# Kernel optimization log

Measured on AMD Instinct MI355X. Metric: run time of the kernel, lower is better.

Reference implementation:

```python
import jax, jax.numpy as jnp
import numpy as np

B = 4096
D = 2048            # in_out_dim
HALF = D // 2       # 1024
MID = 4096          # mid_dim
N_HIDDEN = 5 - 1    # hidden - 1 square layers
MASK = 1            # mask_config


def setup_inputs() -> dict:
    key = jax.random.key(0)
    ks = jax.random.split(key, 8)
    s_in = 1.0 / np.sqrt(HALF)
    s_mid = 1.0 / np.sqrt(MID)
    return {
        "x": jax.random.normal(ks[0], (B, D), dtype=jnp.float32),
        "log_det_J": jnp.zeros((), dtype=jnp.float32),
        "W_in": jax.random.uniform(ks[1], (HALF, MID), jnp.float32, -s_in, s_in),
        "b_in": jax.random.uniform(ks[2], (MID,), jnp.float32, -s_in, s_in),
        "W_h": jax.random.uniform(ks[3], (N_HIDDEN, MID, MID), jnp.float32, -s_mid, s_mid),
        "b_h": jax.random.uniform(ks[4], (N_HIDDEN, MID), jnp.float32, -s_mid, s_mid),
        "W_out": jax.random.uniform(ks[5], (MID, HALF), jnp.float32, -s_mid, s_mid),
        "b_out": jax.random.uniform(ks[6], (HALF,), jnp.float32, -s_mid, s_mid),
    }


def reference(x, log_det_J, W_in, b_in, W_h, b_h, W_out, b_out):
    # reverse=False (sampling mode), mask_config=1
    xr = x.reshape(B, HALF, 2)
    if MASK:
        x1, x2 = xr[:, :, 0], xr[:, :, 1]
    else:
        x1, x2 = xr[:, :, 1], xr[:, :, 0]
    # MLP on the conditioning half
    h = jax.nn.relu(x2 @ W_in + b_in)                  # [B, MID]
    for i in range(N_HIDDEN):
        h = jax.nn.relu(h @ W_h[i] + b_h[i])           # [B, MID]
    out = h @ W_out + b_out                            # [B, HALF]
    x1 = x1 + out
    if MASK:
        y = jnp.stack((x1, x2), axis=2)
    else:
        y = jnp.stack((x2, x1), axis=2)
    return y.reshape(B, D), log_det_J
```

## Files before the change

kernel.cpp:

```cpp
#include <hip/hip_runtime.h>
#include <hip/hip_bf16.h>


#define B_DIM    4096
#define D_DIM    2048
#define HALF_DIM 1024
#define MID_DIM  4096
#define NHID     4

typedef __attribute__((ext_vector_type(8))) short frag_ab;
typedef __attribute__((ext_vector_type(4))) float frag_cd;

#define GAS __attribute__((address_space(1)))
#define LAS __attribute__((address_space(3)))

__device__ __forceinline__ ushort f2bf_rtn(float v) {
    unsigned u = __builtin_bit_cast(unsigned, v);
    unsigned r = u + 0x7FFFu + ((u >> 16) & 1u);
    return (ushort)(r >> 16);
}
__device__ __forceinline__ void split_hilo(float v, ushort& h, ushort& l) {
    h = f2bf_rtn(v);
    float fh = __builtin_bit_cast(float, (unsigned)h << 16);
    l = f2bf_rtn(v - fh);
}

__global__ __launch_bounds__(256) void prep_x2(const float* __restrict__ x,
                                               const float* __restrict__ logd,
                                               ushort* __restrict__ x2h,
                                               ushort* __restrict__ x2l,
                                               float* __restrict__ outLog) {
    int idx = blockIdx.x * 256 + threadIdx.x;
    if (idx == 0) outLog[0] = logd[0];
    float2 v = ((const float2*)x)[idx];
    ushort h, l;
    split_hilo(v.y, h, l);
    x2h[idx] = h; x2l[idx] = l;
}

__global__ __launch_bounds__(256) void transpose_split(const float* __restrict__ in,
                                                       int K, int N,
                                                       ushort* __restrict__ outH,
                                                       ushort* __restrict__ outL) {
    __shared__ float tile[64][65];
    const int n0 = blockIdx.x * 64, k0 = blockIdx.y * 64;
    const int t = threadIdx.x;
    const int c = t & 63, g = t >> 6;
#pragma unroll
    for (int r = 0; r < 16; ++r) {
        int row = g * 16 + r;
        tile[row][c] = in[(size_t)(k0 + row) * N + n0 + c];
    }
    __syncthreads();
#pragma unroll
    for (int r = 0; r < 16; ++r) {
        int nrow = g * 16 + r;
        float v = tile[c][nrow];
        ushort h, l; split_hilo(v, h, l);
        size_t o = (size_t)(n0 + nrow) * K + k0 + c;
        outH[o] = h; outL[o] = l;
    }
}

template <int EPI>
__global__ __launch_bounds__(256, 2) void gemm_hilo(
    const ushort* __restrict__ Ah, const ushort* __restrict__ Al,
    const ushort* __restrict__ Bh, const ushort* __restrict__ Bl,
    const float* __restrict__ bias,
    int M, int N, int K,
    ushort* __restrict__ Ch, ushort* __restrict__ Cl,
    const float* __restrict__ xin, float* __restrict__ yout) {
    __shared__ ushort sAh[4096], sAl[4096], sBh[4096], sBl[4096];
    const int t = threadIdx.x;
    const int w = t >> 6, l = t & 63;
    const int m0 = blockIdx.y * 128, n0 = blockIdx.x * 128;
    const int wr = (w >> 1) * 64, wc = (w & 1) * 64;
    const int lr = l & 15, lk = (l >> 4) * 8;

    frag_cd acc[4][4];
#pragma unroll
    for (int i = 0; i < 4; ++i)
#pragma unroll
        for (int j = 0; j < 4; ++j) acc[i][j] = (frag_cd){0.f, 0.f, 0.f, 0.f};

    float bv[4];
#pragma unroll
    for (int j = 0; j < 4; ++j) bv[j] = bias[n0 + wc + j * 16 + lr];

    const int srow = t >> 2;
    const int scol = (t & 3) * 8;
    const size_t aBase = (size_t)(m0 + srow) * K + scol;
    const size_t bBase = (size_t)(n0 + srow) * K + scol;
    const size_t rstep = (size_t)64 * K;
    const int lo = w * 512;

    for (int k0 = 0; k0 < K; k0 += 32) {
        __syncthreads();
        __builtin_amdgcn_global_load_lds((const GAS void*)(Ah + aBase + k0),         (LAS void*)(sAh + lo),        16, 0, 0);
        __builtin_amdgcn_global_load_lds((const GAS void*)(Ah + aBase + rstep + k0), (LAS void*)(sAh + 2048 + lo), 16, 0, 0);
        __builtin_amdgcn_global_load_lds((const GAS void*)(Al + aBase + k0),         (LAS void*)(sAl + lo),        16, 0, 0);
        __builtin_amdgcn_global_load_lds((const GAS void*)(Al + aBase + rstep + k0), (LAS void*)(sAl + 2048 + lo), 16, 0, 0);
        __builtin_amdgcn_global_load_lds((const GAS void*)(Bh + bBase + k0),         (LAS void*)(sBh + lo),        16, 0, 0);
        __builtin_amdgcn_global_load_lds((const GAS void*)(Bh + bBase + rstep + k0), (LAS void*)(sBh + 2048 + lo), 16, 0, 0);
        __builtin_amdgcn_global_load_lds((const GAS void*)(Bl + bBase + k0),         (LAS void*)(sBl + lo),        16, 0, 0);
        __builtin_amdgcn_global_load_lds((const GAS void*)(Bl + bBase + rstep + k0), (LAS void*)(sBl + 2048 + lo), 16, 0, 0);
        __syncthreads();

        frag_ab fah[4], fal[4], fbh[4], fbl[4];
#pragma unroll
        for (int i = 0; i < 4; ++i) {
            fah[i] = *(const frag_ab*)&sAh[(wr + i * 16 + lr) * 32 + lk];
            fal[i] = *(const frag_ab*)&sAl[(wr + i * 16 + lr) * 32 + lk];
            fbh[i] = *(const frag_ab*)&sBh[(wc + i * 16 + lr) * 32 + lk];
            fbl[i] = *(const frag_ab*)&sBl[(wc + i * 16 + lr) * 32 + lk];
        }
#pragma unroll
        for (int i = 0; i < 4; ++i)
#pragma unroll
            for (int j = 0; j < 4; ++j) {
                acc[i][j] = __builtin_amdgcn_mfma_f32_16x16x32_bf16(fah[i], fbh[j], acc[i][j], 0, 0, 0);
                acc[i][j] = __builtin_amdgcn_mfma_f32_16x16x32_bf16(fah[i], fbl[j], acc[i][j], 0, 0, 0);
                acc[i][j] = __builtin_amdgcn_mfma_f32_16x16x32_bf16(fal[i], fbh[j], acc[i][j], 0, 0, 0);
            }
    }

#pragma unroll
    for (int i = 0; i < 4; ++i) {
        const int rowb = m0 + wr + i * 16 + (l >> 4) * 4;
#pragma unroll
        for (int j = 0; j < 4; ++j) {
            const int col = n0 + wc + j * 16 + lr;
#pragma unroll
            for (int r = 0; r < 4; ++r) {
                float v = acc[i][j][r] + bv[j];
                const int row = rowb + r;
                if (EPI == 0) {
                    v = fmaxf(v, 0.0f);
                    ushort h, lo16; split_hilo(v, h, lo16);
                    size_t o = (size_t)row * N + col;
                    Ch[o] = h; Cl[o] = lo16;
                } else {
                    const float2 xv = *(const float2*)(xin + (size_t)row * D_DIM + 2 * col);
                    float2 yv; yv.x = xv.x + v; yv.y = xv.y;
                    *(float2*)(yout + (size_t)row * D_DIM + 2 * col) = yv;
                }
            }
        }
    }
}

extern "C" void kernel_launch(void* const* d_in, const int* in_sizes, int n_in,
                              void* d_out, int out_size, void* d_ws, size_t ws_size,
                              hipStream_t stream) {
    const float* x     = (const float*)d_in[0];
    const float* logd  = (const float*)d_in[1];
    const float* W_in  = (const float*)d_in[2];
    const float* b_in  = (const float*)d_in[3];
    const float* W_h   = (const float*)d_in[4];
    const float* b_h   = (const float*)d_in[5];
    const float* W_out = (const float*)d_in[6];
    const float* b_out = (const float*)d_in[7];
    float* y = (float*)d_out;

    char* ws = (char*)d_ws;
    ushort* x2h = (ushort*)(ws);
    ushort* x2l = (ushort*)(ws + (size_t)8  * (1 << 20));
    ushort* wth = (ushort*)(ws + (size_t)16 * (1 << 20));
    ushort* wtl = (ushort*)(ws + (size_t)48 * (1 << 20));
    ushort* h0h = (ushort*)(ws + (size_t)80 * (1 << 20));
    ushort* h0l = (ushort*)(ws + (size_t)112 * (1 << 20));
    ushort* h1h = (ushort*)(ws + (size_t)144 * (1 << 20));
    ushort* h1l = (ushort*)(ws + (size_t)176 * (1 << 20));

    prep_x2<<<dim3(B_DIM * HALF_DIM / 256), 256, 0, stream>>>(
        x, logd, x2h, x2l, y + (size_t)B_DIM * D_DIM);

    transpose_split<<<dim3(MID_DIM / 64, HALF_DIM / 64), 256, 0, stream>>>(
        W_in, HALF_DIM, MID_DIM, wth, wtl);
    gemm_hilo<0><<<dim3(MID_DIM / 128, B_DIM / 128), 256, 0, stream>>>(
        x2h, x2l, wth, wtl, b_in, B_DIM, MID_DIM, HALF_DIM, h0h, h0l, nullptr, nullptr);

    ushort *ah = h0h, *al = h0l, *ch = h1h, *cl = h1l;
    for (int i = 0; i < NHID; ++i) {
        transpose_split<<<dim3(MID_DIM / 64, MID_DIM / 64), 256, 0, stream>>>(
            W_h + (size_t)i * MID_DIM * MID_DIM, MID_DIM, MID_DIM, wth, wtl);
        gemm_hilo<0><<<dim3(MID_DIM / 128, B_DIM / 128), 256, 0, stream>>>(
            ah, al, wth, wtl, b_h + (size_t)i * MID_DIM, B_DIM, MID_DIM, MID_DIM,
            ch, cl, nullptr, nullptr);
        ushort* th = ah; ah = ch; ch = th;
        ushort* tl = al; al = cl; cl = tl;
    }

    transpose_split<<<dim3(HALF_DIM / 64, MID_DIM / 64), 256, 0, stream>>>(
        W_out, MID_DIM, HALF_DIM, wth, wtl);
    gemm_hilo<1><<<dim3(HALF_DIM / 128, B_DIM / 128), 256, 0, stream>>>(
        ah, al, wth, wtl, b_out, B_DIM, HALF_DIM, MID_DIM, nullptr, nullptr, x, y);

    (void)in_sizes; (void)n_in; (void)out_size; (void)ws_size;
}
```

Baseline: 2.346 ms.

## Interleave hi/lo bf16 with swizzled layout, 256x256 tiles, double-buffered LDS

Stores the hi and lo bf16 halves interleaved in 32-element k-panels with an XOR swizzle, so one 16-byte load per thread fetches both halves and LDS fragment reads avoid bank conflicts. The square GEMMs move to 256x256 tiles with 512 threads and 8x4 accumulators per wave. Both GEMMs double-buffer LDS so the next k-tile loads while MFMAs run, and they add block-index swizzling for L2 locality plus setprio around the MFMA loops. The larger tile raises register and LDS pressure (128KB LDS per block), which can limit occupancy.

```diff
diff --git a/kernel.cpp b/kernel.cpp
--- a/kernel.cpp
+++ b/kernel.cpp
@@ -27,55 +27,179 @@
 
 __global__ __launch_bounds__(256) void prep_x2(const float* __restrict__ x,
                                                const float* __restrict__ logd,
-                                               ushort* __restrict__ x2h,
-                                               ushort* __restrict__ x2l,
+                                               ushort* __restrict__ x2p,
                                                float* __restrict__ outLog) {
     int idx = blockIdx.x * 256 + threadIdx.x;
     if (idx == 0) outLog[0] = logd[0];
+    int b = idx >> 10, c = idx & 1023;
     float2 v = ((const float2*)x)[idx];
-    ushort h, l;
-    split_hilo(v.y, h, l);
-    x2h[idx] = h; x2l[idx] = l;
+    ushort h, l; split_hilo(v.y, h, l);
+    int kt = c >> 5, w = c & 31;
+    int pos = (w >> 3) ^ (b & 7);
+    size_t base = ((size_t)(b * 32 + kt)) * 64 + (w & 7);
+    x2p[base + pos * 8]       = h;
+    x2p[base + (pos ^ 4) * 8] = l;
 }
 
 __global__ __launch_bounds__(256) void transpose_split(const float* __restrict__ in,
                                                        int K, int N,
-                                                       ushort* __restrict__ outH,
-                                                       ushort* __restrict__ outL) {
+                                                       ushort* __restrict__ outP) {
     __shared__ float tile[64][65];
     const int n0 = blockIdx.x * 64, k0 = blockIdx.y * 64;
     const int t = threadIdx.x;
     const int c = t & 63, g = t >> 6;
 #pragma unroll
-    for (int r = 0; r < 16; ++r) {
-        int row = g * 16 + r;
-        tile[row][c] = in[(size_t)(k0 + row) * N + n0 + c];
-    }
+    for (int r = 0; r < 16; ++r)
+        tile[g * 16 + r][c] = in[(size_t)(k0 + g * 16 + r) * N + n0 + c];
     __syncthreads();
+    const int PK = K >> 5;
 #pragma unroll
     for (int r = 0; r < 16; ++r) {
         int nrow = g * 16 + r;
         float v = tile[c][nrow];
+        int n = n0 + nrow, k = k0 + c;
         ushort h, l; split_hilo(v, h, l);
-        size_t o = (size_t)(n0 + nrow) * K + k0 + c;
-        outH[o] = h; outL[o] = l;
-    }
-}
-
-template <int EPI>
-__global__ __launch_bounds__(256, 2) void gemm_hilo(
-    const ushort* __restrict__ Ah, const ushort* __restrict__ Al,
-    const ushort* __restrict__ Bh, const ushort* __restrict__ Bl,
-    const float* __restrict__ bias,
-    int M, int N, int K,
-    ushort* __restrict__ Ch, ushort* __restrict__ Cl,
-    const float* __restrict__ xin, float* __restrict__ yout) {
-    __shared__ ushort sAh[4096], sAl[4096], sBh[4096], sBl[4096];
+        int kt = k >> 5, w = k & 31;
+        int pos = (w >> 3) ^ (n & 7);
+        size_t base = ((size_t)n * PK + kt) * 64 + (w & 7);
+        outP[base + pos * 8]       = h;
+        outP[base + (pos ^ 4) * 8] = l;
+    }
+}
+
+__global__ __launch_bounds__(512, 2) void gemm8(
+    const ushort* __restrict__ Ap, const ushort* __restrict__ Bp,
+    const float* __restrict__ bias, int K, int N,
+    ushort* __restrict__ Cp) {
+    __shared__ ushort sA[2][16384];
+    __shared__ ushort sB[2][16384];
     const int t = threadIdx.x;
     const int w = t >> 6, l = t & 63;
-    const int m0 = blockIdx.y * 128, n0 = blockIdx.x * 128;
-    const int wr = (w >> 1) * 64, wc = (w & 1) * 64;
-    const int lr = l & 15, lk = (l >> 4) * 8;
+    const int bid = blockIdx.x;
+    const int swz = (bid & 7) * 32 + (bid >> 3);
+    const int bx = swz & 15, by = swz >> 4;
+    const int m0 = by * 256, n0 = bx * 256;
+    const int wr = w >> 2, wc = w & 3;
+    const int lr = l & 15, lc = l >> 4;
+    const int PK = K >> 5, NK = PK;
+
+    const ushort* aSrc = Ap + (size_t)(m0 + (t >> 3)) * (PK * 64) + (t & 7) * 8;
+    const ushort* bSrc = Bp + (size_t)(n0 + (t >> 3)) * (PK * 64) + (t & 7) * 8;
+    const size_t qstep = (size_t)64 * PK * 64;
+    const int ldsBase = w * 512;
+
+#define STAGE8(buf, kt) do {                                                         \
+    const ushort* _as = aSrc + (size_t)(kt) * 64;                                    \
+    const ushort* _bs = bSrc + (size_t)(kt) * 64;                                    \
+    _Pragma("unroll")                                                                \
+    for (int q = 0; q < 4; ++q) {                                                    \
+        __builtin_amdgcn_global_load_lds((const GAS void*)(_as + q * qstep),         \
+                                         (LAS void*)&sA[buf][q * 4096 + ldsBase], 16, 0, 0); \
+        __builtin_amdgcn_global_load_lds((const GAS void*)(_bs + q * qstep),         \
+                                         (LAS void*)&sB[buf][q * 4096 + ldsBase], 16, 0, 0); \
+    } } while (0)
+
+    frag_cd acc[8][4];
+#pragma unroll
+    for (int i = 0; i < 8; ++i)
+#pragma unroll
+        for (int j = 0; j < 4; ++j) acc[i][j] = (frag_cd){0.f, 0.f, 0.f, 0.f};
+
+    float bv[4];
+#pragma unroll
+    for (int j = 0; j < 4; ++j) bv[j] = bias[n0 + wc * 64 + j * 16 + lr];
+
+    STAGE8(0, 0);
+    for (int kt = 0; kt < NK; ++kt) {
+        const int cur = kt & 1;
+        __syncthreads();
+        if (kt + 1 < NK) STAGE8(cur ^ 1, kt + 1);
+
+        frag_ab fbh[4], fbl[4];
+#pragma unroll
+        for (int j = 0; j < 4; ++j) {
+            int row = wc * 64 + j * 16 + lr;
+            int ph = lc ^ (row & 7);
+            fbh[j] = *(const frag_ab*)&sB[cur][row * 64 + ph * 8];
+            fbl[j] = *(const frag_ab*)&sB[cur][row * 64 + (ph ^ 4) * 8];
+        }
+#pragma unroll
+        for (int mh = 0; mh < 2; ++mh) {
+            frag_ab fah[4], fal[4];
+#pragma unroll
+            for (int i = 0; i < 4; ++i) {
+                int row = wr * 128 + mh * 64 + i * 16 + lr;
+                int ph = lc ^ (row & 7);
+                fah[i] = *(const frag_ab*)&sA[cur][row * 64 + ph * 8];
+                fal[i] = *(const frag_ab*)&sA[cur][row * 64 + (ph ^ 4) * 8];
+            }
+            __builtin_amdgcn_s_setprio(1);
+#pragma unroll
+            for (int i = 0; i < 4; ++i)
+#pragma unroll
+                for (int j = 0; j < 4; ++j) {
+                    acc[mh * 4 + i][j] = __builtin_amdgcn_mfma_f32_16x16x32_bf16(fah[i], fbh[j], acc[mh * 4 + i][j], 0, 0, 0);
+                    acc[mh * 4 + i][j] = __builtin_amdgcn_mfma_f32_16x16x32_bf16(fah[i], fbl[j], acc[mh * 4 + i][j], 0, 0, 0);
+                    acc[mh * 4 + i][j] = __builtin_amdgcn_mfma_f32_16x16x32_bf16(fal[i], fbh[j], acc[mh * 4 + i][j], 0, 0, 0);
+                }
+            __builtin_amdgcn_s_setprio(0);
+        }
+    }
+#undef STAGE8
+
+    const int PKo = N >> 5;
+#pragma unroll
+    for (int i = 0; i < 8; ++i) {
+#pragma unroll
+        for (int j = 0; j < 4; ++j) {
+            const int col = n0 + wc * 64 + j * 16 + lr;
+            const int kto = col >> 5, w32 = col & 31;
+            const int e = w32 & 7, ch = w32 >> 3;
+#pragma unroll
+            for (int r = 0; r < 4; ++r) {
+                const int row = m0 + wr * 128 + i * 16 + lc * 4 + r;
+                float v = fmaxf(acc[i][j][r] + bv[j], 0.0f);
+                ushort h, lo16; split_hilo(v, h, lo16);
+                const int pos = ch ^ (row & 7);
+                size_t basec = ((size_t)row * PKo + kto) * 64 + e;
+                Cp[basec + pos * 8]       = h;
+                Cp[basec + (pos ^ 4) * 8] = lo16;
+            }
+        }
+    }
+}
+
+__global__ __launch_bounds__(256, 2) void gemm2(
+    const ushort* __restrict__ Ap, const ushort* __restrict__ Bp,
+    const float* __restrict__ bias, int K, int N,
+    const float* __restrict__ xin, float* __restrict__ yout) {
+    __shared__ ushort sA[2][8192];
+    __shared__ ushort sB[2][8192];
+    const int t = threadIdx.x;
+    const int w = t >> 6, l = t & 63;
+    const int bid = blockIdx.x;
+    const int swz = (bid & 7) * 32 + (bid >> 3);
+    const int bx = swz & 7, by = swz >> 3;
+    const int m0 = by * 128, n0 = bx * 128;
+    const int wr = w >> 1, wc = w & 1;
+    const int lr = l & 15, lc = l >> 4;
+    const int PK = K >> 5, NK = PK;
+
+    const ushort* aSrc = Ap + (size_t)(m0 + (t >> 3)) * (PK * 64) + (t & 7) * 8;
+    const ushort* bSrc = Bp + (size_t)(n0 + (t >> 3)) * (PK * 64) + (t & 7) * 8;
+    const size_t qstep = (size_t)32 * PK * 64;
+    const int ldsBase = w * 512;
+
+#define STAGE2(buf, kt) do {                                                         \
+    const ushort* _as = aSrc + (size_t)(kt) * 64;                                    \
+    const ushort* _bs = bSrc + (size_t)(kt) * 64;                                    \
+    _Pragma("unroll")                                                                \
+    for (int q = 0; q < 4; ++q) {                                                    \
+        __builtin_amdgcn_global_load_lds((const GAS void*)(_as + q * qstep),         \
+                                         (LAS void*)&sA[buf][q * 2048 + ldsBase], 16, 0, 0); \
+        __builtin_amdgcn_global_load_lds((const GAS void*)(_bs + q * qstep),         \
+                                         (LAS void*)&sB[buf][q * 2048 + ldsBase], 16, 0, 0); \
+    } } while (0)
 
     frag_cd acc[4][4];
 #pragma unroll
@@ -85,35 +209,27 @@
 
     float bv[4];
 #pragma unroll
-    for (int j = 0; j < 4; ++j) bv[j] = bias[n0 + wc + j * 16 + lr];
-
-    const int srow = t >> 2;
-    const int scol = (t & 3) * 8;
-    const size_t aBase = (size_t)(m0 + srow) * K + scol;
-    const size_t bBase = (size_t)(n0 + srow) * K + scol;
-    const size_t rstep = (size_t)64 * K;
-    const int lo = w * 512;
-
-    for (int k0 = 0; k0 < K; k0 += 32) {
+    for (int j = 0; j < 4; ++j) bv[j] = bias[n0 + wc * 64 + j * 16 + lr];
+
+    STAGE2(0, 0);
+    for (int kt = 0; kt < NK; ++kt) {
+        const int cur = kt & 1;
         __syncthreads();
-        __builtin_amdgcn_global_load_lds((const GAS void*)(Ah + aBase + k0),         (LAS void*)(sAh + lo),        16, 0, 0);
-        __builtin_amdgcn_global_load_lds((const GAS void*)(Ah + aBase + rstep + k0), (LAS void*)(sAh + 2048 + lo), 16, 0, 0);
-        __builtin_amdgcn_global_load_lds((const GAS void*)(Al + aBase + k0),         (LAS void*)(sAl + lo),        16, 0, 0);
-        __builtin_amdgcn_global_load_lds((const GAS void*)(Al + aBase + rstep + k0), (LAS void*)(sAl + 2048 + lo), 16, 0, 0);
-        __builtin_amdgcn_global_load_lds((const GAS void*)(Bh + bBase + k0),         (LAS void*)(sBh + lo),        16, 0, 0);
-        __builtin_amdgcn_global_load_lds((const GAS void*)(Bh + bBase + rstep + k0), (LAS void*)(sBh + 2048 + lo), 16, 0, 0);
-        __builtin_amdgcn_global_load_lds((const GAS void*)(Bl + bBase + k0),         (LAS void*)(sBl + lo),        16, 0, 0);
-        __builtin_amdgcn_global_load_lds((const GAS void*)(Bl + bBase + rstep + k0), (LAS void*)(sBl + 2048 + lo), 16, 0, 0);
-        __syncthreads();
+        if (kt + 1 < NK) STAGE2(cur ^ 1, kt + 1);
 
         frag_ab fah[4], fal[4], fbh[4], fbl[4];
 #pragma unroll
         for (int i = 0; i < 4; ++i) {
-            fah[i] = *(const frag_ab*)&sAh[(wr + i * 16 + lr) * 32 + lk];
-            fal[i] = *(const frag_ab*)&sAl[(wr + i * 16 + lr) * 32 + lk];
-            fbh[i] = *(const frag_ab*)&sBh[(wc + i * 16 + lr) * 32 + lk];
-            fbl[i] = *(const frag_ab*)&sBl[(wc + i * 16 + lr) * 32 + lk];
-        }
+            int rowa = wr * 64 + i * 16 + lr;
+            int pa = lc ^ (rowa & 7);
+            fah[i] = *(const frag_ab*)&sA[cur][rowa * 64 + pa * 8];
+            fal[i] = *(const frag_ab*)&sA[cur][rowa * 64 + (pa ^ 4) * 8];
+            int rowb = wc * 64 + i * 16 + lr;
+            int pb = lc ^ (rowb & 7);
+            fbh[i] = *(const frag_ab*)&sB[cur][rowb * 64 + pb * 8];
+            fbl[i] = *(const frag_ab*)&sB[cur][rowb * 64 + (pb ^ 4) * 8];
+        }
+        __builtin_amdgcn_s_setprio(1);
 #pragma unroll
         for (int i = 0; i < 4; ++i)
 #pragma unroll
@@ -122,28 +238,22 @@
                 acc[i][j] = __builtin_amdgcn_mfma_f32_16x16x32_bf16(fah[i], fbl[j], acc[i][j], 0, 0, 0);
                 acc[i][j] = __builtin_amdgcn_mfma_f32_16x16x32_bf16(fal[i], fbh[j], acc[i][j], 0, 0, 0);
             }
-    }
+        __builtin_amdgcn_s_setprio(0);
+    }
+#undef STAGE2
 
 #pragma unroll
     for (int i = 0; i < 4; ++i) {
-        const int rowb = m0 + wr + i * 16 + (l >> 4) * 4;
 #pragma unroll
         for (int j = 0; j < 4; ++j) {
-            const int col = n0 + wc + j * 16 + lr;
+            const int col = n0 + wc * 64 + j * 16 + lr;
 #pragma unroll
             for (int r = 0; r < 4; ++r) {
+                const int row = m0 + wr * 64 + i * 16 + lc * 4 + r;
                 float v = acc[i][j][r] + bv[j];
-                const int row = rowb + r;
-                if (EPI == 0) {
-                    v = fmaxf(v, 0.0f);
-                    ushort h, lo16; split_hilo(v, h, lo16);
-                    size_t o = (size_t)row * N + col;
-                    Ch[o] = h; Cl[o] = lo16;
-                } else {
-                    const float2 xv = *(const float2*)(xin + (size_t)row * D_DIM + 2 * col);
-                    float2 yv; yv.x = xv.x + v; yv.y = xv.y;
-                    *(float2*)(yout + (size_t)row * D_DIM + 2 * col) = yv;
-                }
+                const float2 xv = ((const float2*)xin)[(size_t)row * (D_DIM / 2) + col];
+                float2 yv; yv.x = xv.x + v; yv.y = xv.y;
+                ((float2*)yout)[(size_t)row * (D_DIM / 2) + col] = yv;
             }
         }
     }
@@ -163,38 +273,30 @@
     float* y = (float*)d_out;
 
     char* ws = (char*)d_ws;
-    ushort* x2h = (ushort*)(ws);
-    ushort* x2l = (ushort*)(ws + (size_t)8  * (1 << 20));
-    ushort* wth = (ushort*)(ws + (size_t)16 * (1 << 20));
-    ushort* wtl = (ushort*)(ws + (size_t)48 * (1 << 20));
-    ushort* h0h = (ushort*)(ws + (size_t)80 * (1 << 20));
-    ushort* h0l = (ushort*)(ws + (size_t)112 * (1 << 20));
-    ushort* h1h = (ushort*)(ws + (size_t)144 * (1 << 20));
-    ushort* h1l = (ushort*)(ws + (size_t)176 * (1 << 20));
+    ushort* x2p = (ushort*)(ws);
+    ushort* wp  = (ushort*)(ws + (size_t)16  * (1 << 20));
+    ushort* h0  = (ushort*)(ws + (size_t)80  * (1 << 20));
+    ushort* h1  = (ushort*)(ws + (size_t)144 * (1 << 20));
 
     prep_x2<<<dim3(B_DIM * HALF_DIM / 256), 256, 0, stream>>>(
-        x, logd, x2h, x2l, y + (size_t)B_DIM * D_DIM);
+        x, logd, x2p, y + (size_t)B_DIM * D_DIM);
 
     transpose_split<<<dim3(MID_DIM / 64, HALF_DIM / 64), 256, 0, stream>>>(
-        W_in, HALF_DIM, MID_DIM, wth, wtl);
-    gemm_hilo<0><<<dim3(MID_DIM / 128, B_DIM / 128), 256, 0, stream>>>(
-        x2h, x2l, wth, wtl, b_in, B_DIM, MID_DIM, HALF_DIM, h0h, h0l, nullptr, nullptr);
-
-    ushort *ah = h0h, *al = h0l, *ch = h1h, *cl = h1l;
+        W_in, HALF_DIM, MID_DIM, wp);
+    gemm8<<<dim3(256), 512, 0, stream>>>(x2p, wp, b_in, HALF_DIM, MID_DIM, h0);
+
+    ushort *ah = h0, *ch = h1;
     for (int i = 0; i < NHID; ++i) {
         transpose_split<<<dim3(MID_DIM / 64, MID_DIM / 64), 256, 0, stream>>>(
-            W_h + (size_t)i * MID_DIM * MID_DIM, MID_DIM, MID_DIM, wth, wtl);
-        gemm_hilo<0><<<dim3(MID_DIM / 128, B_DIM / 128), 256, 0, stream>>>(
-            ah, al, wth, wtl, b_h + (size_t)i * MID_DIM, B_DIM, MID_DIM, MID_DIM,
-            ch, cl, nullptr, nullptr);
-        ushort* th = ah; ah = ch; ch = th;
-        ushort* tl = al; al = cl; cl = tl;
+            W_h + (size_t)i * MID_DIM * MID_DIM, MID_DIM, MID_DIM, wp);
+        gemm8<<<dim3(256), 512, 0, stream>>>(ah, wp, b_h + (size_t)i * MID_DIM,
+                                             MID_DIM, MID_DIM, ch);
+        ushort* tmp = ah; ah = ch; ch = tmp;
     }
 
     transpose_split<<<dim3(HALF_DIM / 64, MID_DIM / 64), 256, 0, stream>>>(
-        W_out, MID_DIM, HALF_DIM, wth, wtl);
-    gemm_hilo<1><<<dim3(HALF_DIM / 128, B_DIM / 128), 256, 0, stream>>>(
-        ah, al, wth, wtl, b_out, B_DIM, HALF_DIM, MID_DIM, nullptr, nullptr, x, y);
+        W_out, MID_DIM, HALF_DIM, wp);
+    gemm2<<<dim3(256), 256, 0, stream>>>(ah, wp, b_out, MID_DIM, HALF_DIM, x, y);
 
     (void)in_sizes; (void)n_in; (void)out_size; (void)ws_size;
 }
```

New measurement: 1.891 ms. -19.4%, faster.
